# Performance work log

Measured on AMD Instinct MI355X. Metric: run time of the kernel, lower is better.

Reference implementation:

```python
import jax, jax.numpy as jnp
import numpy as np

NEG = -1000000.0  # mask fill value used by the torch module


def setup_inputs() -> dict:
    key = jax.random.key(0)
    kq, kk, kv, km = jax.random.split(key, 4)
    B, Q, K, D = 8, 2048, 2048, 128
    queries = jax.random.normal(kq, (B, Q, D), dtype=jnp.float32)
    keys = jax.random.normal(kk, (B, K, D), dtype=jnp.float32)
    values = jax.random.normal(kv, (B, K, D), dtype=jnp.float32)
    attntion_mask = jax.random.randint(km, (B, K), 0, 2, dtype=jnp.int32)
    return {"queries": queries, "keys": keys, "values": values,
            "attntion_mask": attntion_mask}


def reference(queries, keys, values, attntion_mask):
    d = queries.shape[-1]
    # scores: [B, Q, K]
    scores = jnp.einsum('bqd,bkd->bqk', queries, keys) / jnp.sqrt(
        jnp.asarray(d, dtype=queries.dtype))
    # 2D mask [B, K] broadcasts over the query axis (torch repeat_interleave)
    mask = attntion_mask.astype(bool)[:, None, :]  # [B, 1, K]
    scores = jnp.where(mask, scores, NEG)
    weights = jax.nn.softmax(scores, axis=-1)
    # dropout rate is 0.0 (eval mode) -> identity
    return jnp.einsum('bqk,bkv->bqv', weights, values)
```

## Files before the change

### kernel.cpp

```cpp
#include <hip/hip_runtime.h>
#include <stdint.h>

typedef __attribute__((ext_vector_type(8))) short short8;
typedef __attribute__((ext_vector_type(4))) float f32x4;

#define NB 8
#define NQ 2048
#define NK 2048
#define ND 128
#define SCALE 0.08838834764831845f
#define L2E   1.4426950408889634f
#define FMAXC 10.0f

__device__ __forceinline__ uint32_t pk_bf16(float a, float b) {
  uint32_t ua = __builtin_bit_cast(uint32_t, a);
  uint32_t ub = __builtin_bit_cast(uint32_t, b);
  ua += 0x7FFFu + ((ua >> 16) & 1u);
  ub += 0x7FFFu + ((ub >> 16) & 1u);
  return (ua >> 16) | (ub & 0xFFFF0000u);
}

__device__ __forceinline__ void dma16(const void* g, void* l) {
  __builtin_amdgcn_global_load_lds((const __attribute__((address_space(1))) void*)g,
                                   (__attribute__((address_space(3))) void*)l, 16, 0, 0);
}

__global__ __launch_bounds__(256) void compact_kernel(const int* __restrict__ maskm,
                                                      int* __restrict__ idxArr,
                                                      int* __restrict__ KcArr) {
  __shared__ int cnt;
  const int b = blockIdx.x;
  const int t = threadIdx.x;
  const int lane = t & 63;
  if (t == 0) cnt = 0;
  __syncthreads();
#pragma unroll
  for (int j = 0; j < 8; ++j) {
    int k = t * 8 + j;
    bool bit = maskm[b * NK + k] != 0;
    unsigned long long m = __ballot(bit);
    int pre = __popcll(m & ((1ull << lane) - 1ull));
    int tot = __popcll(m);
    int base = 0;
    if (lane == 0 && tot) base = atomicAdd(&cnt, tot);
    base = __shfl(base, 0);
    if (bit) idxArr[b * NK + base + pre] = k;
  }
  __syncthreads();
  int kc = cnt;
  for (int s = kc + t; s < NK; s += 256) idxArr[b * NK + s] = -1;
  if (t == 0) KcArr[b] = kc;
}

__global__ __launch_bounds__(256) void prep_kernel(const float* __restrict__ v,
                                                   const float* __restrict__ kin,
                                                   ushort* __restrict__ vt,
                                                   ushort* __restrict__ kb,
                                                   const int* __restrict__ idxArr) {
  const int t = threadIdx.x;
  const int bid = blockIdx.x;
  if (bid < 512) {
    __shared__ __align__(16) float tile[4096];
    char* sm = (char*)tile;
    const int b = bid >> 6;
    const int k0 = ((bid >> 1) & 31) << 6;
    const int d0 = (bid & 1) << 6;
#pragma unroll
    for (int i = 0; i < 4; ++i) {
      int id = i * 256 + t;
      int k = id >> 4, c = id & 15;
      int src = idxArr[b * NK + k0 + k];
      uint4 val; val.x = 0u; val.y = 0u; val.z = 0u; val.w = 0u;
      if (src >= 0) val = *(const uint4*)(v + (size_t)(b * NK + src) * ND + d0 + c * 4);
      *(uint4*)(sm + k * 256 + ((c ^ (k & 15)) * 16)) = val;
    }
    __syncthreads();
#pragma unroll
    for (int i = 0; i < 2; ++i) {
      int id = i * 256 + t;
      int d = id >> 3, kc = id & 7;
      uint32_t w[4];
#pragma unroll
      for (int jj = 0; jj < 4; ++jj) {
        int kA = kc * 8 + jj * 2, kB = kA + 1;
        float fa = *(const float*)(sm + kA * 256 + (((d >> 2) ^ (kA & 15)) * 16) + (d & 3) * 4);
        float fb = *(const float*)(sm + kB * 256 + (((d >> 2) ^ (kB & 15)) * 16) + (d & 3) * 4);
        w[jj] = pk_bf16(fa, fb);
      }
      uint4 o; o.x = w[0]; o.y = w[1]; o.z = w[2]; o.w = w[3];
      *(uint4*)(vt + (size_t)(b * ND + d0 + d) * NK + k0 + kc * 8) = o;
    }
  } else {
    int gs = (bid - 512) * 16 + (t >> 4);
    int src = idxArr[gs];
    int col = (t & 15) * 8;
    uint4 u; u.x = 0u; u.y = 0u; u.z = 0u; u.w = 0u;
    if (src >= 0) {
      int b2 = gs >> 11;
      const float* p = kin + (size_t)(b2 * NK + src) * ND + col;
      f32x4 a = *(const f32x4*)p;
      f32x4 c = *(const f32x4*)(p + 4);
      u.x = pk_bf16(a[0], a[1]); u.y = pk_bf16(a[2], a[3]);
      u.z = pk_bf16(c[0], c[1]); u.w = pk_bf16(c[2], c[3]);
    }
    *(uint4*)(kb + (size_t)gs * ND + col) = u;
  }
}

#define LDS_BYTES 73728
__global__ __launch_bounds__(256) void attn_kernel(const float* __restrict__ qm,
                                                   const ushort* __restrict__ kbm,
                                                   const ushort* __restrict__ vtm,
                                                   const int* __restrict__ KcArr,
                                                   ushort* __restrict__ opart,
                                                   float* __restrict__ lpart) {
  __shared__ __align__(16) char sm[LDS_BYTES];
  const int o   = blockIdx.x;
  const int bid = (o & 7) * 64 + (o >> 3);
  const int b   = bid >> 6;
  const int q0  = ((bid >> 1) & 31) << 6;
  const int spl = bid & 1;
  const int t = threadIdx.x;
  const int lane = t & 63;
  const int wave = t >> 6;
  const int r = lane & 15;
  const int quad = lane >> 4;
  const int half = wave >> 1;
  const int qg = wave & 1;

  const int Kc   = KcArr[b];
  const int n_it = (Kc + 127) >> 7;
  const int CH   = n_it << 5;

  uint32_t koff[4], voff[4];
#pragma unroll
  for (int j = 0; j < 4; ++j) {
    int i = wave * 4 + j;
    int rho = i * 4 + (lane >> 4);
    int ck = (lane & 15) ^ (rho & 15);
    int krow = (spl * 2 + (rho >> 5)) * CH + (rho & 31);
    koff[j] = (uint32_t)(b * NK + krow) * ND + ck * 8;
    int rv = i * 16 + (lane >> 2);
    int cv = (lane & 3) ^ (rv & 3);
    voff[j] = (uint32_t)(b * ND + (rv & 127)) * NK + (spl * 2 + (rv >> 7)) * CH + cv * 8;
  }

  short8 qf[2][4];
#pragma unroll
  for (int qt = 0; qt < 2; ++qt)
#pragma unroll
    for (int ks = 0; ks < 4; ++ks) {
      const float* p = qm + (size_t)(b * NQ + q0 + qg * 32 + qt * 16 + r) * ND + ks * 32 + quad * 8;
      f32x4 a = *(const f32x4*)p;
      f32x4 c = *(const f32x4*)(p + 4);
      uint4 u;
      u.x = pk_bf16(a[0], a[1]); u.y = pk_bf16(a[2], a[3]);
      u.z = pk_bf16(c[0], c[1]); u.w = pk_bf16(c[2], c[3]);
      qf[qt][ks] = __builtin_bit_cast(short8, u);
    }

  f32x4 oacc[2][8];
#pragma unroll
  for (int qt = 0; qt < 2; ++qt)
#pragma unroll
    for (int dt = 0; dt < 8; ++dt) oacc[qt][dt] = (f32x4){0.f, 0.f, 0.f, 0.f};
  float l_[2] = {0.f, 0.f};

  char* const pbase = sm + 65536 + wave * 2048;

  const int lim0 = Kc - (spl * 2 + half) * CH - quad * 4;

#pragma unroll
  for (int j = 0; j < 4; ++j) {
    dma16(kbm + koff[j], sm + wave * 4096 + j * 1024);
    dma16(vtm + voff[j], sm + 32768 + wave * 4096 + j * 1024);
  }

  for (int it = 0; it < n_it; ++it) {
    const int cur = it & 1;
    char* const kcur = sm + cur * 16384;
    char* const vcur = sm + 32768 + cur * 16384;
    char* const knxt = sm + (cur ^ 1) * 16384;
    char* const vnxt = sm + 32768 + (cur ^ 1) * 16384;

    __syncthreads();

    if (it < n_it - 1) {
      const uint32_t kadd = (uint32_t)(it + 1) * 32 * ND;
      const uint32_t vadd = (uint32_t)(it + 1) * 32;
#pragma unroll
      for (int j = 0; j < 4; ++j) {
        dma16(kbm + koff[j] + kadd, knxt + wave * 4096 + j * 1024);
        dma16(vtm + voff[j] + vadd, vnxt + wave * 4096 + j * 1024);
      }
    }

    short8 kf[2][4];
#pragma unroll
    for (int mt = 0; mt < 2; ++mt)
#pragma unroll
      for (int ks = 0; ks < 4; ++ks)
        kf[mt][ks] = *(const short8*)(kcur + half * 8192 + (mt * 16 + r) * 256 + (((ks * 4 + quad) ^ r) * 16));
    f32x4 st[2][2];
#pragma unroll
    for (int mt = 0; mt < 2; ++mt)
#pragma unroll
      for (int qt = 0; qt < 2; ++qt) {
        f32x4 acc = (f32x4){0.f, 0.f, 0.f, 0.f};
#pragma unroll
        for (int ks = 0; ks < 4; ++ks)
          acc = __builtin_amdgcn_mfma_f32_16x16x32_bf16(kf[mt][ks], qf[qt][ks], acc, 0, 0, 0);
        st[mt][qt] = acc;
      }

    const float C1 = SCALE * L2E;
    const float C2 = -FMAXC * L2E;
    const int rem = lim0 - it * 32;
#pragma unroll
    for (int qt = 0; qt < 2; ++qt) {
      float p[2][4]; float ps = 0.f;
#pragma unroll
      for (int mt = 0; mt < 2; ++mt) {
        const int rm = rem - mt * 16;
        float t0 = (rm > 0) ? fmaf(st[mt][qt][0], C1, C2) : -2.0e6f;
        float t1 = (rm > 1) ? fmaf(st[mt][qt][1], C1, C2) : -2.0e6f;
        float t2 = (rm > 2) ? fmaf(st[mt][qt][2], C1, C2) : -2.0e6f;
        float t3 = (rm > 3) ? fmaf(st[mt][qt][3], C1, C2) : -2.0e6f;
        p[mt][0] = exp2f(t0); p[mt][1] = exp2f(t1);
        p[mt][2] = exp2f(t2); p[mt][3] = exp2f(t3);
        ps += p[mt][0] + p[mt][1] + p[mt][2] + p[mt][3];
      }
      ps += __shfl_xor(ps, 16);
      ps += __shfl_xor(ps, 32);
      l_[qt] += ps;
#pragma unroll
      for (int mt = 0; mt < 2; ++mt) {
        uint2 w; w.x = pk_bf16(p[mt][0], p[mt][1]); w.y = pk_bf16(p[mt][2], p[mt][3]);
        *(uint2*)(pbase + (qt * 16 + r) * 64 + (((mt * 4 + quad) ^ (r & 6)) * 8)) = w;
      }
    }

    short8 pf[2];
#pragma unroll
    for (int qt = 0; qt < 2; ++qt)
      pf[qt] = *(const short8*)(pbase + (qt * 16 + r) * 64 + (((quad * 2) ^ (r & 6)) * 8));
#pragma unroll
    for (int dt = 0; dt < 8; ++dt) {
      short8 vf = *(const short8*)(vcur + half * 8192 + (dt * 16 + r) * 64 + ((quad ^ (r & 3)) * 16));
#pragma unroll
      for (int qt = 0; qt < 2; ++qt)
        oacc[qt][dt] = __builtin_amdgcn_mfma_f32_16x16x32_bf16(vf, pf[qt], oacc[qt][dt], 0, 0, 0);
    }
  }

  __syncthreads();
  float* xch = (float*)(sm + qg * 17408) + lane * 68;
  if (half == 1) {
    xch[0] = l_[0]; xch[1] = l_[1];
#pragma unroll
    for (int qt = 0; qt < 2; ++qt)
#pragma unroll
      for (int dt = 0; dt < 8; ++dt)
        *(f32x4*)(xch + 4 + (qt * 8 + dt) * 4) = oacc[qt][dt];
  }
  __syncthreads();
  if (half == 0) {
#pragma unroll
    for (int qt = 0; qt < 2; ++qt) {
      const int qrow = b * NQ + q0 + qg * 32 + qt * 16 + r;
      float lsum = l_[qt] + xch[qt];
      if (quad == 0) lpart[spl * NB * NQ + qrow] = lsum;
#pragma unroll
      for (int dt = 0; dt < 8; ++dt) {
        f32x4 o1 = *(const f32x4*)(xch + 4 + (qt * 8 + dt) * 4);
        f32x4 ov = oacc[qt][dt] + o1;
        uint2 w; w.x = pk_bf16(ov[0], ov[1]); w.y = pk_bf16(ov[2], ov[3]);
        *(uint2*)(opart + (size_t)spl * NB * NQ * ND + (size_t)qrow * ND + dt * 16 + quad * 4) = w;
      }
    }
  }
}

__global__ __launch_bounds__(256) void merge_kernel(const ushort* __restrict__ opart,
                                                    const float* __restrict__ lpart,
                                                    float* __restrict__ outm) {
  const int gid = blockIdx.x * 256 + threadIdx.x;
  const int row = gid >> 4;
  const int d0 = (gid & 15) << 3;
  const size_t off = (size_t)row * ND + d0;
  uint4 u0 = *(const uint4*)(opart + off);
  uint4 u1 = *(const uint4*)(opart + (size_t)NB * NQ * ND + off);
  float inv = 1.0f / (lpart[row] + lpart[NB * NQ + row]);
  f32x4 lo, hi;
  uint32_t w;
#define UP(u, dst0, dst1) w = (u); dst0 = __builtin_bit_cast(float, w << 16); \
                          dst1 = __builtin_bit_cast(float, w & 0xFFFF0000u);
  float a0,a1,b0,b1;
  UP(u0.x, a0, a1) UP(u1.x, b0, b1) lo[0] = (a0 + b0) * inv; lo[1] = (a1 + b1) * inv;
  UP(u0.y, a0, a1) UP(u1.y, b0, b1) lo[2] = (a0 + b0) * inv; lo[3] = (a1 + b1) * inv;
  UP(u0.z, a0, a1) UP(u1.z, b0, b1) hi[0] = (a0 + b0) * inv; hi[1] = (a1 + b1) * inv;
  UP(u0.w, a0, a1) UP(u1.w, b0, b1) hi[2] = (a0 + b0) * inv; hi[3] = (a1 + b1) * inv;
#undef UP
  *(f32x4*)(outm + off) = lo;
  *(f32x4*)(outm + off + 4) = hi;
}

extern "C" void kernel_launch(void* const* d_in, const int* in_sizes, int n_in,
                              void* d_out, int out_size, void* d_ws, size_t ws_size,
                              hipStream_t stream) {
  const float* q   = (const float*)d_in[0];
  const float* k   = (const float*)d_in[1];
  const float* v   = (const float*)d_in[2];
  const int*   msk = (const int*)d_in[3];
  float* out = (float*)d_out;
  ushort* kb = (ushort*)d_ws;
  ushort* vt = kb + (size_t)NB * NK * ND;
  ushort* op = vt + (size_t)NB * NK * ND;
  float*  lp = (float*)(op + 2 * (size_t)NB * NQ * ND);
  int* idxA  = (int*)(lp + 2 * (size_t)NB * NQ);
  int* kcA   = idxA + (size_t)NB * NK;

  compact_kernel<<<NB, 256, 0, stream>>>(msk, idxA, kcA);
  prep_kernel<<<1536, 256, 0, stream>>>(v, k, vt, kb, idxA);
  attn_kernel<<<512, 256, 0, stream>>>(q, kb, vt, kcA, op, lp);
  merge_kernel<<<1024, 256, 0, stream>>>(op, lp, out);
}
```

Before: 109.6 us.

## Use 512-thread blocks with 128-query tiles and four-way key split

Each attention block now runs 8 waves covering 128 queries, and the compacted keys are split four ways instead of two, giving more waves per block that share K/V loads. The softmax is split into a mask-free fast path plus a masked path used only for the last partial tile, and the row-sum shuffles move out of the inner loop to the epilogue. The merge kernel now sums four partial bf16 outputs. The cost is a larger partial-output workspace, more merge traffic and more extra rounding from partial results stored in bf16.

Result: slower. 114.7 us (+4.7%).

```diff
diff --git a/kernel.cpp b/kernel.cpp
--- a/kernel.cpp
+++ b/kernel.cpp
@@ -107,8 +107,39 @@
   }
 }
 
+template <bool MASKED>
+__device__ __forceinline__ void do_softmax(const f32x4 st[2], float& l_,
+                                           char* pbase, int r, int quad, int rem) {
+  const float C1 = SCALE * L2E;
+  const float C2 = -FMAXC * L2E;
+  float p[2][4]; float ps = 0.f;
+#pragma unroll
+  for (int mt = 0; mt < 2; ++mt) {
+    float t0 = fmaf(st[mt][0], C1, C2);
+    float t1 = fmaf(st[mt][1], C1, C2);
+    float t2 = fmaf(st[mt][2], C1, C2);
+    float t3 = fmaf(st[mt][3], C1, C2);
+    if (MASKED) {
+      const int rm = rem - mt * 16;
+      t0 = (rm > 0) ? t0 : -2.0e6f;
+      t1 = (rm > 1) ? t1 : -2.0e6f;
+      t2 = (rm > 2) ? t2 : -2.0e6f;
+      t3 = (rm > 3) ? t3 : -2.0e6f;
+    }
+    p[mt][0] = exp2f(t0); p[mt][1] = exp2f(t1);
+    p[mt][2] = exp2f(t2); p[mt][3] = exp2f(t3);
+    ps += p[mt][0] + p[mt][1] + p[mt][2] + p[mt][3];
+  }
+  l_ += ps;
+#pragma unroll
+  for (int mt = 0; mt < 2; ++mt) {
+    uint2 w; w.x = pk_bf16(p[mt][0], p[mt][1]); w.y = pk_bf16(p[mt][2], p[mt][3]);
+    *(uint2*)(pbase + r * 64 + (((mt * 4 + quad) ^ (r & 6)) * 8)) = w;
+  }
+}
+
 #define LDS_BYTES 73728
-__global__ __launch_bounds__(256) void attn_kernel(const float* __restrict__ qm,
+__global__ __launch_bounds__(512) void attn_kernel(const float* __restrict__ qm,
                                                    const ushort* __restrict__ kbm,
                                                    const ushort* __restrict__ vtm,
                                                    const int* __restrict__ KcArr,
@@ -118,24 +149,24 @@
   const int o   = blockIdx.x;
   const int bid = (o & 7) * 64 + (o >> 3);
   const int b   = bid >> 6;
-  const int q0  = ((bid >> 1) & 31) << 6;
-  const int spl = bid & 1;
+  const int q0  = ((bid >> 2) & 15) << 7;
+  const int spl = bid & 3;
   const int t = threadIdx.x;
   const int lane = t & 63;
   const int wave = t >> 6;
   const int r = lane & 15;
   const int quad = lane >> 4;
-  const int half = wave >> 1;
-  const int qg = wave & 1;
+  const int half = wave >> 2;
+  const int qg = wave & 3;
 
   const int Kc   = KcArr[b];
-  const int n_it = (Kc + 127) >> 7;
+  const int n_it = (Kc + 255) >> 8;
   const int CH   = n_it << 5;
 
-  uint32_t koff[4], voff[4];
-#pragma unroll
-  for (int j = 0; j < 4; ++j) {
-    int i = wave * 4 + j;
+  uint32_t koff[2], voff[2];
+#pragma unroll
+  for (int j = 0; j < 2; ++j) {
+    int i = wave * 2 + j;
     int rho = i * 4 + (lane >> 4);
     int ck = (lane & 15) ^ (rho & 15);
     int krow = (spl * 2 + (rho >> 5)) * CH + (rho & 31);
@@ -143,6 +174,12 @@
     int rv = i * 16 + (lane >> 2);
     int cv = (lane & 3) ^ (rv & 3);
     voff[j] = (uint32_t)(b * ND + (rv & 127)) * NK + (spl * 2 + (rv >> 7)) * CH + cv * 8;
+  }
+
+#pragma unroll
+  for (int j = 0; j < 2; ++j) {
+    dma16(kbm + koff[j], sm + (wave * 2 + j) * 1024);
+    dma16(vtm + voff[j], sm + 32768 + (wave * 2 + j) * 1024);
   }
 
   short8 qf[2][4];
@@ -166,21 +203,15 @@
     for (int dt = 0; dt < 8; ++dt) oacc[qt][dt] = (f32x4){0.f, 0.f, 0.f, 0.f};
   float l_[2] = {0.f, 0.f};
 
-  char* const pbase = sm + 65536 + wave * 2048;
-
-  const int lim0 = Kc - (spl * 2 + half) * CH - quad * 4;
-
-#pragma unroll
-  for (int j = 0; j < 4; ++j) {
-    dma16(kbm + koff[j], sm + wave * 4096 + j * 1024);
-    dma16(vtm + voff[j], sm + 32768 + wave * 4096 + j * 1024);
-  }
+  char* const pbase = sm + 65536 + wave * 1024;
+
+  const int vlim0 = Kc - (spl * 2 + half) * CH;
 
   for (int it = 0; it < n_it; ++it) {
     const int cur = it & 1;
     char* const kcur = sm + cur * 16384;
+    char* const knxt = sm + (cur ^ 1) * 16384;
     char* const vcur = sm + 32768 + cur * 16384;
-    char* const knxt = sm + (cur ^ 1) * 16384;
     char* const vnxt = sm + 32768 + (cur ^ 1) * 16384;
 
     __syncthreads();
@@ -189,61 +220,39 @@
       const uint32_t kadd = (uint32_t)(it + 1) * 32 * ND;
       const uint32_t vadd = (uint32_t)(it + 1) * 32;
 #pragma unroll
-      for (int j = 0; j < 4; ++j) {
-        dma16(kbm + koff[j] + kadd, knxt + wave * 4096 + j * 1024);
-        dma16(vtm + voff[j] + vadd, vnxt + wave * 4096 + j * 1024);
+      for (int j = 0; j < 2; ++j) {
+        dma16(kbm + koff[j] + kadd, knxt + (wave * 2 + j) * 1024);
+        dma16(vtm + voff[j] + vadd, vnxt + (wave * 2 + j) * 1024);
       }
     }
 
-    short8 kf[2][4];
-#pragma unroll
-    for (int mt = 0; mt < 2; ++mt)
+    f32x4 st[2][2];
+#pragma unroll
+    for (int mt = 0; mt < 2; ++mt) {
+      short8 kf[4];
 #pragma unroll
       for (int ks = 0; ks < 4; ++ks)
-        kf[mt][ks] = *(const short8*)(kcur + half * 8192 + (mt * 16 + r) * 256 + (((ks * 4 + quad) ^ r) * 16));
-    f32x4 st[2][2];
-#pragma unroll
-    for (int mt = 0; mt < 2; ++mt)
+        kf[ks] = *(const short8*)(kcur + half * 8192 + (mt * 16 + r) * 256 + (((ks * 4 + quad) ^ r) * 16));
 #pragma unroll
       for (int qt = 0; qt < 2; ++qt) {
         f32x4 acc = (f32x4){0.f, 0.f, 0.f, 0.f};
 #pragma unroll
         for (int ks = 0; ks < 4; ++ks)
-          acc = __builtin_amdgcn_mfma_f32_16x16x32_bf16(kf[mt][ks], qf[qt][ks], acc, 0, 0, 0);
+          acc = __builtin_amdgcn_mfma_f32_16x16x32_bf16(kf[ks], qf[qt][ks], acc, 0, 0, 0);
         st[mt][qt] = acc;
       }
-
-    const float C1 = SCALE * L2E;
-    const float C2 = -FMAXC * L2E;
-    const int rem = lim0 - it * 32;
+    }
+
+    const int vlim = vlim0 - it * 32;
+    short8 pf[2];
 #pragma unroll
     for (int qt = 0; qt < 2; ++qt) {
-      float p[2][4]; float ps = 0.f;
-#pragma unroll
-      for (int mt = 0; mt < 2; ++mt) {
-        const int rm = rem - mt * 16;
-        float t0 = (rm > 0) ? fmaf(st[mt][qt][0], C1, C2) : -2.0e6f;
-        float t1 = (rm > 1) ? fmaf(st[mt][qt][1], C1, C2) : -2.0e6f;
-        float t2 = (rm > 2) ? fmaf(st[mt][qt][2], C1, C2) : -2.0e6f;
-        float t3 = (rm > 3) ? fmaf(st[mt][qt][3], C1, C2) : -2.0e6f;
-        p[mt][0] = exp2f(t0); p[mt][1] = exp2f(t1);
-        p[mt][2] = exp2f(t2); p[mt][3] = exp2f(t3);
-        ps += p[mt][0] + p[mt][1] + p[mt][2] + p[mt][3];
-      }
-      ps += __shfl_xor(ps, 16);
-      ps += __shfl_xor(ps, 32);
-      l_[qt] += ps;
-#pragma unroll
-      for (int mt = 0; mt < 2; ++mt) {
-        uint2 w; w.x = pk_bf16(p[mt][0], p[mt][1]); w.y = pk_bf16(p[mt][2], p[mt][3]);
-        *(uint2*)(pbase + (qt * 16 + r) * 64 + (((mt * 4 + quad) ^ (r & 6)) * 8)) = w;
-      }
-    }
-
-    short8 pf[2];
-#pragma unroll
-    for (int qt = 0; qt < 2; ++qt)
-      pf[qt] = *(const short8*)(pbase + (qt * 16 + r) * 64 + (((quad * 2) ^ (r & 6)) * 8));
+      f32x4 s2[2] = { st[0][qt], st[1][qt] };
+      if (vlim >= 32) do_softmax<false>(s2, l_[qt], pbase, r, quad, 0);
+      else            do_softmax<true >(s2, l_[qt], pbase, r, quad, vlim - quad * 4);
+      pf[qt] = *(const short8*)(pbase + r * 64 + (((quad * 2) ^ (r & 6)) * 8));
+    }
+
 #pragma unroll
     for (int dt = 0; dt < 8; ++dt) {
       short8 vf = *(const short8*)(vcur + half * 8192 + (dt * 16 + r) * 64 + ((quad ^ (r & 3)) * 16));
@@ -268,8 +277,10 @@
 #pragma unroll
     for (int qt = 0; qt < 2; ++qt) {
       const int qrow = b * NQ + q0 + qg * 32 + qt * 16 + r;
-      float lsum = l_[qt] + xch[qt];
-      if (quad == 0) lpart[spl * NB * NQ + qrow] = lsum;
+      float ls = l_[qt] + xch[qt];
+      ls += __shfl_xor(ls, 16);
+      ls += __shfl_xor(ls, 32);
+      if (quad == 0) lpart[spl * NB * NQ + qrow] = ls;
 #pragma unroll
       for (int dt = 0; dt < 8; ++dt) {
         f32x4 o1 = *(const f32x4*)(xch + 4 + (qt * 8 + dt) * 4);
@@ -288,19 +299,27 @@
   const int row = gid >> 4;
   const int d0 = (gid & 15) << 3;
   const size_t off = (size_t)row * ND + d0;
-  uint4 u0 = *(const uint4*)(opart + off);
-  uint4 u1 = *(const uint4*)(opart + (size_t)NB * NQ * ND + off);
-  float inv = 1.0f / (lpart[row] + lpart[NB * NQ + row]);
+  float acc[8];
+#pragma unroll
+  for (int j = 0; j < 8; ++j) acc[j] = 0.f;
+  float lsum = 0.f;
+#pragma unroll
+  for (int s = 0; s < 4; ++s) {
+    uint4 u = *(const uint4*)(opart + (size_t)s * NB * NQ * ND + off);
+    lsum += lpart[s * NB * NQ + row];
+    acc[0] += __builtin_bit_cast(float, u.x << 16);
+    acc[1] += __builtin_bit_cast(float, u.x & 0xFFFF0000u);
+    acc[2] += __builtin_bit_cast(float, u.y << 16);
+    acc[3] += __builtin_bit_cast(float, u.y & 0xFFFF0000u);
+    acc[4] += __builtin_bit_cast(float, u.z << 16);
+    acc[5] += __builtin_bit_cast(float, u.z & 0xFFFF0000u);
+    acc[6] += __builtin_bit_cast(float, u.w << 16);
+    acc[7] += __builtin_bit_cast(float, u.w & 0xFFFF0000u);
+  }
+  float inv = 1.0f / lsum;
   f32x4 lo, hi;
-  uint32_t w;
-#define UP(u, dst0, dst1) w = (u); dst0 = __builtin_bit_cast(float, w << 16); \
-                          dst1 = __builtin_bit_cast(float, w & 0xFFFF0000u);
-  float a0,a1,b0,b1;
-  UP(u0.x, a0, a1) UP(u1.x, b0, b1) lo[0] = (a0 + b0) * inv; lo[1] = (a1 + b1) * inv;
-  UP(u0.y, a0, a1) UP(u1.y, b0, b1) lo[2] = (a0 + b0) * inv; lo[3] = (a1 + b1) * inv;
-  UP(u0.z, a0, a1) UP(u1.z, b0, b1) hi[0] = (a0 + b0) * inv; hi[1] = (a1 + b1) * inv;
-  UP(u0.w, a0, a1) UP(u1.w, b0, b1) hi[2] = (a0 + b0) * inv; hi[3] = (a1 + b1) * inv;
-#undef UP
+  lo[0] = acc[0] * inv; lo[1] = acc[1] * inv; lo[2] = acc[2] * inv; lo[3] = acc[3] * inv;
+  hi[0] = acc[4] * inv; hi[1] = acc[5] * inv; hi[2] = acc[6] * inv; hi[3] = acc[7] * inv;
   *(f32x4*)(outm + off) = lo;
   *(f32x4*)(outm + off + 4) = hi;
 }
@@ -316,12 +335,12 @@
   ushort* kb = (ushort*)d_ws;
   ushort* vt = kb + (size_t)NB * NK * ND;
   ushort* op = vt + (size_t)NB * NK * ND;
-  float*  lp = (float*)(op + 2 * (size_t)NB * NQ * ND);
-  int* idxA  = (int*)(lp + 2 * (size_t)NB * NQ);
+  float*  lp = (float*)(op + 4 * (size_t)NB * NQ * ND);
+  int* idxA  = (int*)(lp + 4 * (size_t)NB * NQ);
   int* kcA   = idxA + (size_t)NB * NK;
 
   compact_kernel<<<NB, 256, 0, stream>>>(msk, idxA, kcA);
   prep_kernel<<<1536, 256, 0, stream>>>(v, k, vt, kb, idxA);
-  attn_kernel<<<512, 256, 0, stream>>>(q, kb, vt, kcA, op, lp);
+  attn_kernel<<<512, 512, 0, stream>>>(q, kb, vt, kcA, op, lp);
   merge_kernel<<<1024, 256, 0, stream>>>(op, lp, out);
 }
```
